# Kernel tuning notes

Hardware: AMD Instinct MI355X
Metric: run time of the kernel (lower is better)

The kernel has to match this reference:

```python
import jax, jax.numpy as jnp
import numpy as np

N = 50000       # nodes
E = 500000      # edges (before self-loops)
F_IN = 128      # node feature dim
F_E = 16        # edge feature dim
H = 8           # heads (conv1, conv2)
C1 = 32         # 256 // 8
C2 = 16         # 128 // 8
OUT = 1         # conv3 output channels (1 head, concat=False)
NS = 0.2        # leaky_relu negative slope
EPS = 1e-5      # batchnorm eps


def setup_inputs() -> dict:
    key = jax.random.key(0)
    ks = jax.random.split(key, 32)
    r = lambda k, s: jax.random.normal(k, s, jnp.float32) * 0.1
    inp = {
        'x': jax.random.normal(ks[0], (N, F_IN), jnp.float32),
        'edge_index': jax.random.randint(ks[1], (2, E), 0, N, jnp.int32),
        'edge_attr': jax.random.normal(ks[2], (E, F_E), jnp.float32),
        # conv1 (share_weights=True -> single lin)
        'W1': r(ks[3], (F_IN, H * C1)), 'b1': jnp.zeros((H * C1,), jnp.float32),
        'We1': r(ks[4], (F_E, H * C1)), 'att1': r(ks[5], (H, C1)),
        'bo1': jnp.zeros((H * C1,), jnp.float32),
        'g1': jnp.ones((H * C1,), jnp.float32), 'bt1': jnp.zeros((H * C1,), jnp.float32),
        # conv2 (share_weights=True)
        'W2': r(ks[6], (H * C1, H * C2)), 'b2': jnp.zeros((H * C2,), jnp.float32),
        'We2': r(ks[7], (F_E, H * C2)), 'att2': r(ks[8], (H, C2)),
        'bo2': jnp.zeros((H * C2,), jnp.float32),
        'g2': jnp.ones((H * C2,), jnp.float32), 'bt2': jnp.zeros((H * C2,), jnp.float32),
        # conv3 (share_weights=False -> separate lin_l / lin_r; 1 head, concat=False)
        'W3l': r(ks[9], (H * C2, OUT)), 'b3l': jnp.zeros((OUT,), jnp.float32),
        'W3r': r(ks[10], (H * C2, OUT)), 'b3r': jnp.zeros((OUT,), jnp.float32),
        'We3': r(ks[11], (F_E, OUT)), 'att3': r(ks[12], (1, OUT)),
        'bo3': jnp.zeros((OUT,), jnp.float32),
    }
    return inp


def _gatv2(x, src, dst, eattr, Wl, bl, Wr, br, We, att, bo, heads, ch, concat):
    """One GATv2Conv layer (PyG semantics), edges already include self-loops."""
    n = x.shape[0]
    xl = (x @ Wl + bl).reshape(n, heads, ch)              # source transform
    xr = (x @ Wr + br).reshape(n, heads, ch)              # target transform
    e = (eattr @ We).reshape(-1, heads, ch)               # edge transform (no bias)
    m = xl[src] + xr[dst] + e                             # [Etot, H, C]
    logit = jnp.einsum('ehc,hc->eh', jax.nn.leaky_relu(m, NS), att)
    lmax = jax.ops.segment_max(logit, dst, num_segments=n)
    ex = jnp.exp(logit - lmax[dst])
    denom = jax.ops.segment_sum(ex, dst, num_segments=n)
    alpha = ex / (denom[dst] + 1e-16)                     # segment softmax over dst
    out = jax.ops.segment_sum(alpha[:, :, None] * xl[src], dst, num_segments=n)
    out = out.reshape(n, heads * ch) if concat else out.mean(axis=1)
    return out + bo


def _bn(x, g, b):
    mu = x.mean(axis=0)
    var = ((x - mu) ** 2).mean(axis=0)
    return g * (x - mu) * jax.lax.rsqrt(var + EPS) + b


def reference(x, edge_index, edge_attr, W1, b1, We1, att1, bo1, g1, bt1,
              W2, b2, We2, att2, bo2, g2, bt2,
              W3l, b3l, W3r, b3r, We3, att3, bo3):
    n = x.shape[0]
    # add_self_loops=True with fill_value='mean' for edge_attr (PyG default)
    loop = jnp.arange(n, dtype=edge_index.dtype)
    src = jnp.concatenate([edge_index[0], loop])
    dst = jnp.concatenate([edge_index[1], loop])
    ea = jnp.concatenate([edge_attr,
                          jnp.broadcast_to(edge_attr.mean(axis=0), (n, edge_attr.shape[1]))], axis=0)

    h = _gatv2(x, src, dst, ea, W1, b1, W1, b1, We1, att1, bo1, H, C1, True)
    h = jax.nn.elu(_bn(h, g1, bt1))
    h = _gatv2(h, src, dst, ea, W2, b2, W2, b2, We2, att2, bo2, H, C2, True)
    h = jax.nn.elu(_bn(h, g2, bt2))
    out = _gatv2(h, src, dst, ea, W3l, b3l, W3r, b3r, We3, att3, bo3, 1, OUT, False)
    return out  # [N, 1]
```

## Files before the change

### kernel.cpp

```cpp
#include <hip/hip_runtime.h>

typedef unsigned short u16;
typedef __attribute__((ext_vector_type(4))) float f32x4;
typedef __attribute__((ext_vector_type(2))) float f32x2;
typedef __attribute__((ext_vector_type(8))) short bf16x8;

constexpr int Nn  = 50000;
constexpr int Ee  = 500000;
constexpr int ET  = Nn + Ee;
constexpr int FIN = 128;
constexpr int FE  = 16;
constexpr int Hh  = 8;
constexpr int C1  = 32, HC1 = 256;
constexpr int C2  = 16, HC2 = 128;
constexpr float NS  = 0.2f;
constexpr float EPS = 1e-5f;
constexpr float LOG2E = 1.44269504088896340736f;
constexpr int ATTN_BLOCKS = 2048;
constexpr int NWAVES = ATTN_BLOCKS * 4;

__device__ __forceinline__ float b2f(u16 u) { return __uint_as_float(((unsigned)u) << 16); }
__device__ __forceinline__ u16 f2b(float f) {
  unsigned u = __float_as_uint(f);
  u += 0x7FFF + ((u >> 16) & 1);
  return (u16)(u >> 16);
}

template <int RED>
__device__ __forceinline__ float red_sum(float v) {
  v += __int_as_float(__builtin_amdgcn_update_dpp(0, __float_as_int(v), 0xB1, 0xF, 0xF, true));
  v += __int_as_float(__builtin_amdgcn_update_dpp(0, __float_as_int(v), 0x4E, 0xF, 0xF, true));
  v += __int_as_float(__builtin_amdgcn_update_dpp(0, __float_as_int(v), 0x141, 0xF, 0xF, true));
  if constexpr (RED == 16)
    v += __int_as_float(__builtin_amdgcn_update_dpp(0, __float_as_int(v), 0x140, 0xF, 0xF, true));
  return v;
}

__global__ void k_init(int* __restrict__ deg, int* __restrict__ cursor, float* __restrict__ ea_mean) {
  int t = blockIdx.x * 256 + threadIdx.x;
  int stride = gridDim.x * 256;
  for (int i = t; i < Nn; i += stride) { deg[i] = 0; cursor[i] = 0; }
  if (t < FE) ea_mean[t] = 0.f;
}

__global__ void k_deg_mean(const int* __restrict__ ei, const float* __restrict__ ea,
                           int* __restrict__ deg, float* __restrict__ ea_mean) {
  int t = threadIdx.x;
  int e = blockIdx.x * 256 + t;
  if (e < ET) {
    int d = (e < Ee) ? ei[Ee + e] : (e - Ee);
    if ((unsigned)d >= (unsigned)Nn) d = 0;
    atomicAdd(&deg[d], 1);
  }
  __shared__ float s[256];
  int f  = t & 15;
  int r0 = (t >> 4) + blockIdx.x * 16;
  float acc = 0.f;
  for (int r = r0; r < Ee; r += gridDim.x * 16) acc += ea[r * FE + f];
  s[t] = acc;
  __syncthreads();
  if (t < 16) {
    float v = 0.f;
    for (int r = 0; r < 16; r++) v += s[r * 16 + t];
    atomicAdd(&ea_mean[t], v * (1.f / Ee));
  }
}

__global__ __launch_bounds__(1024) void k_scan(const int* __restrict__ deg, int* __restrict__ rowptr) {
  const int T = 1024;
  int t = threadIdx.x;
  const int CH = (Nn + T - 1) / T;
  int base = t * CH;
  int sum = 0;
  for (int i = 0; i < CH; i++) {
    int idx = base + i;
    if (idx < Nn) sum += deg[idx];
  }
  __shared__ int s[T];
  s[t] = sum;
  __syncthreads();
  for (int off = 1; off < T; off <<= 1) {
    int v = (t >= off) ? s[t - off] : 0;
    __syncthreads();
    s[t] += v;
    __syncthreads();
  }
  int run = (t == 0) ? 0 : s[t - 1];
  for (int i = 0; i < CH; i++) {
    int idx = base + i;
    if (idx < Nn) { rowptr[idx] = run; run += deg[idx]; }
  }
  if (t == T - 1) rowptr[Nn] = run;
}

__global__ void k_scatter(const int* __restrict__ ei, const int* __restrict__ rowptr,
                          int* __restrict__ cursor, int2* __restrict__ epack) {
  int e = blockIdx.x * 256 + threadIdx.x;
  if (e >= ET) return;
  if (e < 4) epack[ET + e] = make_int2(0, Ee);
  int s, d;
  if (e < Ee) { s = ei[e]; d = ei[Ee + e]; } else { s = d = e - Ee; }
  if ((unsigned)s >= (unsigned)Nn) s = 0;
  if ((unsigned)d >= (unsigned)Nn) d = 0;
  int pos = rowptr[d] + atomicAdd(&cursor[d], 1);
  epack[pos] = make_int2(s, e);
}

template <int WPN>
__global__ __launch_bounds__(256) void k_bn_coef_red(
    const float4* __restrict__ bnpart, const float* __restrict__ g,
    const float* __restrict__ bt, float2* __restrict__ coef) {
  constexpr int NW = NWAVES / WPN;
  int b = blockIdx.x;
  int w = b >> 6, lane = b & 63;
  int t = threadIdx.x;
  float4 s = make_float4(0.f, 0.f, 0.f, 0.f);
  for (int k = t; k < NW; k += 256) {
    float4 p = bnpart[(size_t)(k * WPN + w) * 64 + lane];
    s.x += p.x; s.y += p.y; s.z += p.z; s.w += p.w;
  }
  __shared__ float4 red[256];
  red[t] = s;
  __syncthreads();
  for (int off = 128; off > 0; off >>= 1) {
    if (t < off) {
      float4 o = red[t + off];
      red[t].x += o.x; red[t].y += o.y; red[t].z += o.z; red[t].w += o.w;
    }
    __syncthreads();
  }
  if (t == 0) {
    float4 tot = red[0];
    int c0 = w * 128 + lane * 2;
    float mu0 = tot.x * (1.f / Nn);
    float var0 = tot.y * (1.f / Nn) - mu0 * mu0;
    float sc0 = g[c0] * rsqrtf(var0 + EPS);
    coef[c0] = make_float2(sc0, bt[c0] - sc0 * mu0);
    float mu1 = tot.z * (1.f / Nn);
    float var1 = tot.w * (1.f / Nn) - mu1 * mu1;
    float sc1 = g[c0 + 1] * rsqrtf(var1 + EPS);
    coef[c0 + 1] = make_float2(sc1, bt[c0 + 1] - sc1 * mu1);
  }
}

template <int KK, int NN, typename AT, bool FUSE>
__global__ __launch_bounds__(256) void k_gemm_mfma(const AT* __restrict__ A, const float* __restrict__ W,
                                                   const float* __restrict__ bias, u16* __restrict__ C,
                                                   const float2* __restrict__ coef, int M) {
  int nblk = gridDim.x;
  int n = blockIdx.x;
  int q = nblk >> 3, r = nblk & 7;
  int xcd = n & 7, idx = n >> 3;
  int np = (xcd < r ? xcd * (q + 1) : r * (q + 1) + (xcd - r) * q) + idx;
  constexpr int XB = NN / 64;
  int col0 = (np % XB) * 64;
  int row0 = (np / XB) * 64;

  constexpr int WT = KK + 8;
  __shared__ u16 Wt[64 * WT];
  int tid = threadIdx.x;
  for (int idx2 = tid; idx2 < KK * 64; idx2 += 256) {
    int k = idx2 >> 6, c = idx2 & 63;
    Wt[c * WT + k] = f2b(W[(size_t)k * NN + col0 + c]);
  }
  __syncthreads();
  int lane = tid & 63;
  int w = tid >> 6;
  int mr = lane & 15, quad = lane >> 4;
  int row = row0 + w * 16 + mr;
  f32x4 acc[4];
#pragma unroll
  for (int t = 0; t < 4; t++) acc[t] = (f32x4){0.f, 0.f, 0.f, 0.f};
  union Frag { bf16x8 v; u16 u[8]; };
  for (int kb = 0; kb < KK; kb += 32) {
    Frag a;
    if (row < M) {
      if constexpr (sizeof(AT) == 4) {
        const float* ap = (const float*)&A[(size_t)row * KK + kb + quad * 8];
        float4 a0 = *reinterpret_cast<const float4*>(ap);
        float4 a1 = *reinterpret_cast<const float4*>(ap + 4);
        a.u[0] = f2b(a0.x); a.u[1] = f2b(a0.y); a.u[2] = f2b(a0.z); a.u[3] = f2b(a0.w);
        a.u[4] = f2b(a1.x); a.u[5] = f2b(a1.y); a.u[6] = f2b(a1.z); a.u[7] = f2b(a1.w);
      } else {
        a.v = *reinterpret_cast<const bf16x8*>(&A[(size_t)row * KK + kb + quad * 8]);
        if constexpr (FUSE) {
          int k0 = kb + quad * 8;
#pragma unroll
          for (int j = 0; j < 8; j++) {
            float2 c2 = coef[k0 + j];
            float y = b2f(a.u[j]) * c2.x + c2.y;
            y = y > 0.f ? y : __expf(y) - 1.f;
            a.u[j] = f2b(y);
          }
        }
      }
    } else {
#pragma unroll
      for (int j = 0; j < 8; j++) a.u[j] = 0;
    }
#pragma unroll
    for (int t = 0; t < 4; t++) {
      const bf16x8* bp = reinterpret_cast<const bf16x8*>(&Wt[(t * 16 + mr) * WT + kb + quad * 8]);
      acc[t] = __builtin_amdgcn_mfma_f32_16x16x32_bf16(a.v, *bp, acc[t], 0, 0, 0);
    }
  }
  int orow = row0 + w * 16 + quad * 4;
#pragma unroll
  for (int t = 0; t < 4; t++) {
    int col = col0 + t * 16 + mr;
    float bs = bias[col];
#pragma unroll
    for (int r2 = 0; r2 < 4; r2++) {
      int rr = orow + r2;
      if (rr < M) C[(size_t)rr * NN + col] = f2b(acc[t][r2] + bs);
    }
  }
}

template <int HC, int C, int WPN>
__global__ __launch_bounds__(256) void k_node_attn(
    const int* __restrict__ rowptr, const int2* __restrict__ epack,
    const u16* __restrict__ xl, const float* __restrict__ We, const float* __restrict__ att,
    const float* __restrict__ edge_attr, const float* __restrict__ ea_mean,
    const float* __restrict__ bo, u16* __restrict__ out,
    float4* __restrict__ bnpart) {
  __shared__ float sea[4][2][4][16];
  int lane = threadIdx.x & 63;
  int widx = threadIdx.x >> 6;
  int gwid = (blockIdx.x << 2) + widx;
  int nwaves = gridDim.x << 2;
  int w = gwid % WPN;
  int i0 = gwid / WPN;
  int istride = nwaves / WPN;
  int c0 = w * 128 + lane * 2;
  f32x2 w2[FE];
#pragma unroll
  for (int k = 0; k < FE; k++) {
    float2 t = *reinterpret_cast<const float2*>(&We[k * HC + c0]);
    w2[k] = (f32x2){t.x, t.y};
  }
  float at0 = att[c0] * LOG2E, at1 = att[c0 + 1] * LOG2E;
  f32x2 ews2 = {0.f, 0.f};
#pragma unroll
  for (int k = 0; k < FE; k++) ews2 += ea_mean[k] * w2[k];
  float b0 = bo[c0], b1 = bo[c0 + 1];
  constexpr int RED = C / 2;
  constexpr int UN = 4;

  auto stage = [&](const int2* sep, int buf) {
    int y01 = (lane & 4) ? sep[1].y : sep[0].y;
    int y23 = (lane & 4) ? sep[3].y : sep[2].y;
    int eidv = (lane & 8) ? y23 : y01;
    int ec = (eidv < Ee) ? eidv : 0;
    const float* src = edge_attr + (size_t)ec * FE + (lane & 3) * 4;
    if (lane < 16) {
      __builtin_amdgcn_global_load_lds(
          (const __attribute__((address_space(1))) unsigned int*)src,
          (__attribute__((address_space(3))) unsigned int*)&sea[widx][buf][0][0],
          16, 0, 0);
    }
  };
  auto ea_dot_lds = [&](int eid, int buf, int jj) -> f32x2 {
    if (eid < Ee) {
      const float4* ep = reinterpret_cast<const float4*>(&sea[widx][buf][jj][0]);
      f32x2 a = {0.f, 0.f};
#pragma unroll
      for (int k4 = 0; k4 < 4; k4++) {
        float4 u = ep[k4];
        a += u.x * w2[4 * k4 + 0];
        a += u.y * w2[4 * k4 + 1];
        a += u.z * w2[4 * k4 + 2];
        a += u.w * w2[4 * k4 + 3];
      }
      return a;
    }
    return ews2;
  };

  float bs0 = 0.f, bq0 = 0.f, bs1 = 0.f, bq1 = 0.f;
  if (i0 >= Nn) {
    bnpart[(size_t)gwid * 64 + lane] = make_float4(0.f, 0.f, 0.f, 0.f);
    return;
  }
  int p0 = __builtin_amdgcn_readfirstlane(rowptr[i0]);
  int p1 = __builtin_amdgcn_readfirstlane(rowptr[i0 + 1]);
  ushort2 xdr = *reinterpret_cast<const ushort2*>(&xl[(size_t)i0 * HC + c0]);

  for (int i = i0; i < Nn;) {
    int inext = i + istride;
    int np0 = 0, np1 = 0;
    ushort2 nxdr = make_ushort2(0, 0);
    if (inext < Nn) {
      np0 = __builtin_amdgcn_readfirstlane(rowptr[inext]);
      np1 = __builtin_amdgcn_readfirstlane(rowptr[inext + 1]);
      nxdr = *reinterpret_cast<const ushort2*>(&xl[(size_t)inext * HC + c0]);
    }
    f32x2 xd = (f32x2){b2f(xdr.x), b2f(xdr.y)};
    int nb = (p1 - p0 + UN - 1) >> 2;
    float m = -1e30f, l = 0.f;
    f32x2 acc = {0.f, 0.f};

    int2 se[UN];
#pragma unroll
    for (int j = 0; j < UN; j++) se[j] = epack[p0 + j];
    stage(se, 0);

    int pb = p0;
    for (int b = 0; b < nb; b++) {
      int buf = b & 1;
      asm volatile("s_waitcnt vmcnt(0)" ::: "memory");
      int sA[UN], eA[UN];
#pragma unroll
      for (int j = 0; j < UN; j++) {
        sA[j] = __builtin_amdgcn_readfirstlane(se[j].x);
        eA[j] = __builtin_amdgcn_readfirstlane(se[j].y);
      }
      ushort2 xr[UN];
#pragma unroll
      for (int j = 0; j < UN; j++)
        xr[j] = *reinterpret_cast<const ushort2*>(&xl[(size_t)sA[j] * HC + c0]);
      int pn = pb + UN;
      bool more = pn < p1;
      if (more) {
#pragma unroll
        for (int j = 0; j < UN; j++) se[j] = epack[pn + j];
      }
      f32x2 xs[UN];
      float part[UN];
#pragma unroll
      for (int j = 0; j < UN; j++) {
        f32x2 ew = ea_dot_lds(eA[j], buf, j);
        xs[j] = (f32x2){b2f(xr[j].x), b2f(xr[j].y)};
        f32x2 t = xs[j] + xd + ew;
        f32x2 tn = t * NS;
        float lk0 = fmaxf(t.x, tn.x), lk1 = fmaxf(t.y, tn.y);
        float pt = lk0 * at0 + lk1 * at1;
        pt = red_sum<RED>(pt);
        part[j] = (pb + j < p1) ? pt : -1e30f;
      }
      if (more) stage(se, buf ^ 1);
      float mn = m;
#pragma unroll
      for (int j = 0; j < UN; j++) mn = fmaxf(mn, part[j]);
      float sc = __builtin_amdgcn_exp2f(m - mn);
      float a[UN], asum = 0.f;
      f32x2 ax = {0.f, 0.f};
#pragma unroll
      for (int j = 0; j < UN; j++) {
        a[j] = __builtin_amdgcn_exp2f(part[j] - mn);
        asum += a[j];
        ax += a[j] * xs[j];
      }
      l = l * sc + asum;
      acc = acc * sc + ax;
      m = mn;
      pb = pn;
    }
    float inv = 1.f / (l + 1e-16f);
    f32x2 v = {acc.x * inv + b0, acc.y * inv + b1};
    u16 r0 = f2b(v.x), r1 = f2b(v.y);
    ushort2 ru; ru.x = r0; ru.y = r1;
    *reinterpret_cast<ushort2*>(&out[(size_t)i * HC + c0]) = ru;
    float v0 = b2f(r0), v1 = b2f(r1);
    bs0 += v0; bq0 += v0 * v0; bs1 += v1; bq1 += v1 * v1;
    i = inext; p0 = np0; p1 = np1; xdr = nxdr;
  }
  bnpart[(size_t)gwid * 64 + lane] = make_float4(bs0, bq0, bs1, bq1);
}

__global__ __launch_bounds__(256) void k_gemv3(const u16* __restrict__ h2,
                                               const float2* __restrict__ coef,
                                               const float* __restrict__ W3l, const float* __restrict__ b3l,
                                               const float* __restrict__ W3r, const float* __restrict__ b3r,
                                               float* __restrict__ xl3, float* __restrict__ xr3) {
  int lane = threadIdx.x & 63;
  int i = (blockIdx.x << 2) + (threadIdx.x >> 6);
  if (i >= Nn) return;
  float2 ca = coef[lane], cb = coef[64 + lane];
  float a = b2f(h2[(long)i * HC2 + lane]) * ca.x + ca.y;
  a = a > 0.f ? a : __expf(a) - 1.f;
  float b = b2f(h2[(long)i * HC2 + 64 + lane]) * cb.x + cb.y;
  b = b > 0.f ? b : __expf(b) - 1.f;
  float pl = a * W3l[lane] + b * W3l[64 + lane];
  float pr = a * W3r[lane] + b * W3r[64 + lane];
  for (int o = 1; o < 64; o <<= 1) { pl += __shfl_xor(pl, o); pr += __shfl_xor(pr, o); }
  if (lane == 0) { xl3[i] = pl + b3l[0]; xr3[i] = pr + b3r[0]; }
}

__global__ __launch_bounds__(256) void k_final3(
    const int* __restrict__ rowptr, const int2* __restrict__ epack,
    const float* __restrict__ xl3, const float* __restrict__ xr3,
    const float* __restrict__ We3, const float* __restrict__ att3,
    const float* __restrict__ edge_attr, const float* __restrict__ ea_mean,
    const float* __restrict__ bo3, float* __restrict__ out) {
  int t = threadIdx.x;
  int lane16 = t & 15;
  int i = blockIdx.x * 16 + (t >> 4);
  if (i >= Nn) return;
  float we[FE];
#pragma unroll
  for (int k4 = 0; k4 < 4; k4++) {
    float4 u = reinterpret_cast<const float4*>(We3)[k4];
    we[4 * k4] = u.x; we[4 * k4 + 1] = u.y; we[4 * k4 + 2] = u.z; we[4 * k4 + 3] = u.w;
  }
  float at = att3[0];
  float ews = 0.f;
#pragma unroll
  for (int k = 0; k < FE; k++) ews += ea_mean[k] * we[k];
  float xd = xr3[i];
  int p0 = rowptr[i], p1 = rowptr[i + 1];
  float m = -1e30f, l = 0.f, o = 0.f;
  for (int p = p0 + lane16; p < p1; p += 16) {
    int2 se = epack[p];
    int s = se.x, eid = se.y;
    float ew;
    if (eid < Ee) {
      const float4* ep = reinterpret_cast<const float4*>(&edge_attr[(size_t)eid * FE]);
      ew = 0.f;
#pragma unroll
      for (int k4 = 0; k4 < 4; k4++) {
        float4 u = ep[k4];
        ew += u.x * we[4 * k4] + u.y * we[4 * k4 + 1] + u.z * we[4 * k4 + 2] + u.w * we[4 * k4 + 3];
      }
    } else ew = ews;
    float xsv = xl3[s];
    float tt = xsv + xd + ew;
    float v = tt > 0.f ? tt : NS * tt;
    float logit = v * at;
    float mn = fmaxf(m, logit);
    float sc = __expf(m - mn);
    float a = __expf(logit - mn);
    l = l * sc + a;
    o = o * sc + a * xsv;
    m = mn;
  }
  float M = m;
#pragma unroll
  for (int off = 1; off < 16; off <<= 1) M = fmaxf(M, __shfl_xor(M, off));
  float adj = __expf(m - M);
  float lw = l * adj, ow = o * adj;
#pragma unroll
  for (int off = 1; off < 16; off <<= 1) { lw += __shfl_xor(lw, off); ow += __shfl_xor(ow, off); }
  if (lane16 == 0) out[i] = ow / (lw + 1e-16f) + bo3[0];
}

extern "C" void kernel_launch(void* const* d_in, const int* in_sizes, int n_in,
                              void* d_out, int out_size, void* d_ws, size_t ws_size,
                              hipStream_t stream) {
  const float* x    = (const float*)d_in[0];
  const int*   ei   = (const int*)d_in[1];
  const float* ea   = (const float*)d_in[2];
  const float* W1   = (const float*)d_in[3];
  const float* b1   = (const float*)d_in[4];
  const float* We1  = (const float*)d_in[5];
  const float* att1 = (const float*)d_in[6];
  const float* bo1  = (const float*)d_in[7];
  const float* g1   = (const float*)d_in[8];
  const float* bt1  = (const float*)d_in[9];
  const float* W2   = (const float*)d_in[10];
  const float* b2   = (const float*)d_in[11];
  const float* We2  = (const float*)d_in[12];
  const float* att2 = (const float*)d_in[13];
  const float* bo2  = (const float*)d_in[14];
  const float* g2   = (const float*)d_in[15];
  const float* bt2  = (const float*)d_in[16];
  const float* W3l  = (const float*)d_in[17];
  const float* b3l  = (const float*)d_in[18];
  const float* W3r  = (const float*)d_in[19];
  const float* b3r  = (const float*)d_in[20];
  const float* We3  = (const float*)d_in[21];
  const float* att3 = (const float*)d_in[22];
  const float* bo3  = (const float*)d_in[23];
  float* out = (float*)d_out;

  char* ws = (char*)d_ws;
  size_t off = 0;
  auto alloc = [&](size_t bytes) -> void* {
    void* p = ws + off;
    off = (off + bytes + 255) & ~(size_t)255;
    return p;
  };
  int*    deg     = (int*)alloc((size_t)Nn * 4);
  int*    rowptr  = (int*)alloc((size_t)(Nn + 1) * 4);
  int*    cursor  = (int*)alloc((size_t)Nn * 4);
  int2*   epack   = (int2*)alloc((size_t)(ET + 4) * 8);
  float*  ea_mean = (float*)alloc((size_t)FE * 4);
  float2* bncoef  = (float2*)alloc(256 * 8);
  float*  xl3     = (float*)alloc((size_t)Nn * 4);
  float*  xr3     = (float*)alloc((size_t)Nn * 4);
  u16*    xlA     = (u16*)alloc((size_t)Nn * 256 * 2);
  u16*    hB      = (u16*)alloc((size_t)Nn * 256 * 2);
  float4* bnpart  = (float4*)alloc((size_t)NWAVES * 64 * 16);

  k_init<<<512, 256, 0, stream>>>(deg, cursor, ea_mean);
  k_deg_mean<<<(ET + 255) / 256, 256, 0, stream>>>(ei, ea, deg, ea_mean);
  k_scan<<<1, 1024, 0, stream>>>(deg, rowptr);
  k_scatter<<<(ET + 255) / 256, 256, 0, stream>>>(ei, rowptr, cursor, epack);

  const int RB = (Nn + 63) / 64;

  k_gemm_mfma<FIN, HC1, float, false><<<(HC1 / 64) * RB, 256, 0, stream>>>(
      x, W1, b1, xlA, nullptr, Nn);
  k_node_attn<HC1, C1, 2><<<ATTN_BLOCKS, 256, 0, stream>>>(rowptr, epack, xlA, We1, att1,
                                                           ea, ea_mean, bo1, hB, bnpart);
  k_bn_coef_red<2><<<128, 256, 0, stream>>>(bnpart, g1, bt1, bncoef);

  k_gemm_mfma<HC1, HC2, u16, true><<<(HC2 / 64) * RB, 256, 0, stream>>>(
      hB, W2, b2, xlA, bncoef, Nn);
  k_node_attn<HC2, C2, 1><<<ATTN_BLOCKS, 256, 0, stream>>>(rowptr, epack, xlA, We2, att2,
                                                           ea, ea_mean, bo2, hB, bnpart);
  k_bn_coef_red<1><<<64, 256, 0, stream>>>(bnpart, g2, bt2, bncoef);

  k_gemv3<<<(Nn + 3) / 4, 256, 0, stream>>>(hB, bncoef, W3l, b3l, W3r, b3r, xl3, xr3);
  k_final3<<<(Nn + 15) / 16, 256, 0, stream>>>(rowptr, epack, xl3, xr3, We3, att3,
                                               ea, ea_mean, bo3, out);
}
```

Before: 646.0 us.

## Precompute conv3 edge projections and deepen edge-index prefetch in attention

The conv3 edge term (edge_attr · We3) is now computed once per edge inside the degree/mean pass and stored as a scalar array. The final kernel then reads one float per edge instead of gathering 64 bytes of edge features. The attention kernel prefetches edge-index packs two blocks ahead and stages the next block's edge features earlier, so index loads overlap with the gathers. The epack padding is enlarged to cover the deeper prefetch, and the row pointers are no longer forced to scalar registers at load time. This adds a 2 MB workspace array plus extra registers in the attention loop.

```diff
diff --git a/kernel.cpp b/kernel.cpp
--- a/kernel.cpp
+++ b/kernel.cpp
@@ -18,6 +18,7 @@
 constexpr float LOG2E = 1.44269504088896340736f;
 constexpr int ATTN_BLOCKS = 2048;
 constexpr int NWAVES = ATTN_BLOCKS * 4;
+constexpr int EPAD = 12;
 
 __device__ __forceinline__ float b2f(u16 u) { return __uint_as_float(((unsigned)u) << 16); }
 __device__ __forceinline__ u16 f2b(float f) {
@@ -44,7 +45,9 @@
 }
 
 __global__ void k_deg_mean(const int* __restrict__ ei, const float* __restrict__ ea,
-                           int* __restrict__ deg, float* __restrict__ ea_mean) {
+                           const float* __restrict__ We3,
+                           int* __restrict__ deg, float* __restrict__ ea_mean,
+                           float* __restrict__ ew3) {
   int t = threadIdx.x;
   int e = blockIdx.x * 256 + t;
   if (e < ET) {
@@ -54,9 +57,15 @@
   }
   __shared__ float s[256];
   int f  = t & 15;
+  float w3 = We3[f];
   int r0 = (t >> 4) + blockIdx.x * 16;
   float acc = 0.f;
-  for (int r = r0; r < Ee; r += gridDim.x * 16) acc += ea[r * FE + f];
+  for (int r = r0; r < Ee; r += gridDim.x * 16) {
+    float v = ea[r * FE + f];
+    acc += v;
+    float d3 = red_sum<16>(v * w3);
+    if (f == 0) ew3[r] = d3;
+  }
   s[t] = acc;
   __syncthreads();
   if (t < 16) {
@@ -97,7 +106,7 @@
                           int* __restrict__ cursor, int2* __restrict__ epack) {
   int e = blockIdx.x * 256 + threadIdx.x;
   if (e >= ET) return;
-  if (e < 4) epack[ET + e] = make_int2(0, Ee);
+  if (e < EPAD) epack[ET + e] = make_int2(0, Ee);
   int s, d;
   if (e < Ee) { s = ei[e]; d = ei[Ee + e]; } else { s = d = e - Ee; }
   if ((unsigned)s >= (unsigned)Nn) s = 0;
@@ -282,8 +291,7 @@
     bnpart[(size_t)gwid * 64 + lane] = make_float4(0.f, 0.f, 0.f, 0.f);
     return;
   }
-  int p0 = __builtin_amdgcn_readfirstlane(rowptr[i0]);
-  int p1 = __builtin_amdgcn_readfirstlane(rowptr[i0 + 1]);
+  int p0 = rowptr[i0], p1 = rowptr[i0 + 1];
   ushort2 xdr = *reinterpret_cast<const ushort2*>(&xl[(size_t)i0 * HC + c0]);
 
   for (int i = i0; i < Nn;) {
@@ -291,8 +299,8 @@
     int np0 = 0, np1 = 0;
     ushort2 nxdr = make_ushort2(0, 0);
     if (inext < Nn) {
-      np0 = __builtin_amdgcn_readfirstlane(rowptr[inext]);
-      np1 = __builtin_amdgcn_readfirstlane(rowptr[inext + 1]);
+      np0 = rowptr[inext];
+      np1 = rowptr[inext + 1];
       nxdr = *reinterpret_cast<const ushort2*>(&xl[(size_t)inext * HC + c0]);
     }
     f32x2 xd = (f32x2){b2f(xdr.x), b2f(xdr.y)};
@@ -300,30 +308,35 @@
     float m = -1e30f, l = 0.f;
     f32x2 acc = {0.f, 0.f};
 
-    int2 se[UN];
-#pragma unroll
-    for (int j = 0; j < UN; j++) se[j] = epack[p0 + j];
-    stage(se, 0);
+    int2 seC[UN], seN[UN];
+#pragma unroll
+    for (int j = 0; j < UN; j++) seC[j] = epack[p0 + j];
+    stage(seC, 0);
+#pragma unroll
+    for (int j = 0; j < UN; j++) seN[j] = epack[p0 + UN + j];
 
     int pb = p0;
     for (int b = 0; b < nb; b++) {
       int buf = b & 1;
       asm volatile("s_waitcnt vmcnt(0)" ::: "memory");
+      int pn = pb + UN;
+      bool more = pn < p1;
+      if (more) stage(seN, buf ^ 1);
       int sA[UN], eA[UN];
 #pragma unroll
       for (int j = 0; j < UN; j++) {
-        sA[j] = __builtin_amdgcn_readfirstlane(se[j].x);
-        eA[j] = __builtin_amdgcn_readfirstlane(se[j].y);
+        sA[j] = __builtin_amdgcn_readfirstlane(seC[j].x);
+        eA[j] = __builtin_amdgcn_readfirstlane(seC[j].y);
       }
       ushort2 xr[UN];
 #pragma unroll
       for (int j = 0; j < UN; j++)
         xr[j] = *reinterpret_cast<const ushort2*>(&xl[(size_t)sA[j] * HC + c0]);
-      int pn = pb + UN;
-      bool more = pn < p1;
+#pragma unroll
+      for (int j = 0; j < UN; j++) seC[j] = seN[j];
       if (more) {
 #pragma unroll
-        for (int j = 0; j < UN; j++) se[j] = epack[pn + j];
+        for (int j = 0; j < UN; j++) seN[j] = epack[pn + UN + j];
       }
       f32x2 xs[UN];
       float part[UN];
@@ -338,7 +351,6 @@
         pt = red_sum<RED>(pt);
         part[j] = (pb + j < p1) ? pt : -1e30f;
       }
-      if (more) stage(se, buf ^ 1);
       float mn = m;
 #pragma unroll
       for (int j = 0; j < UN; j++) mn = fmaxf(mn, part[j]);
@@ -391,38 +403,23 @@
     const int* __restrict__ rowptr, const int2* __restrict__ epack,
     const float* __restrict__ xl3, const float* __restrict__ xr3,
     const float* __restrict__ We3, const float* __restrict__ att3,
-    const float* __restrict__ edge_attr, const float* __restrict__ ea_mean,
+    const float* __restrict__ ew3, const float* __restrict__ ea_mean,
     const float* __restrict__ bo3, float* __restrict__ out) {
   int t = threadIdx.x;
   int lane16 = t & 15;
   int i = blockIdx.x * 16 + (t >> 4);
   if (i >= Nn) return;
-  float we[FE];
-#pragma unroll
-  for (int k4 = 0; k4 < 4; k4++) {
-    float4 u = reinterpret_cast<const float4*>(We3)[k4];
-    we[4 * k4] = u.x; we[4 * k4 + 1] = u.y; we[4 * k4 + 2] = u.z; we[4 * k4 + 3] = u.w;
-  }
   float at = att3[0];
   float ews = 0.f;
 #pragma unroll
-  for (int k = 0; k < FE; k++) ews += ea_mean[k] * we[k];
+  for (int k = 0; k < FE; k++) ews += ea_mean[k] * We3[k];
   float xd = xr3[i];
   int p0 = rowptr[i], p1 = rowptr[i + 1];
   float m = -1e30f, l = 0.f, o = 0.f;
   for (int p = p0 + lane16; p < p1; p += 16) {
     int2 se = epack[p];
     int s = se.x, eid = se.y;
-    float ew;
-    if (eid < Ee) {
-      const float4* ep = reinterpret_cast<const float4*>(&edge_attr[(size_t)eid * FE]);
-      ew = 0.f;
-#pragma unroll
-      for (int k4 = 0; k4 < 4; k4++) {
-        float4 u = ep[k4];
-        ew += u.x * we[4 * k4] + u.y * we[4 * k4 + 1] + u.z * we[4 * k4 + 2] + u.w * we[4 * k4 + 3];
-      }
-    } else ew = ews;
+    float ew = (eid < Ee) ? ew3[eid] : ews;
     float xsv = xl3[s];
     float tt = xsv + xd + ew;
     float v = tt > 0.f ? tt : NS * tt;
@@ -483,8 +480,9 @@
   int*    deg     = (int*)alloc((size_t)Nn * 4);
   int*    rowptr  = (int*)alloc((size_t)(Nn + 1) * 4);
   int*    cursor  = (int*)alloc((size_t)Nn * 4);
-  int2*   epack   = (int2*)alloc((size_t)(ET + 4) * 8);
+  int2*   epack   = (int2*)alloc((size_t)(ET + EPAD) * 8);
   float*  ea_mean = (float*)alloc((size_t)FE * 4);
+  float*  ew3     = (float*)alloc((size_t)Ee * 4);
   float2* bncoef  = (float2*)alloc(256 * 8);
   float*  xl3     = (float*)alloc((size_t)Nn * 4);
   float*  xr3     = (float*)alloc((size_t)Nn * 4);
@@ -493,7 +491,7 @@
   float4* bnpart  = (float4*)alloc((size_t)NWAVES * 64 * 16);
 
   k_init<<<512, 256, 0, stream>>>(deg, cursor, ea_mean);
-  k_deg_mean<<<(ET + 255) / 256, 256, 0, stream>>>(ei, ea, deg, ea_mean);
+  k_deg_mean<<<(ET + 255) / 256, 256, 0, stream>>>(ei, ea, We3, deg, ea_mean, ew3);
   k_scan<<<1, 1024, 0, stream>>>(deg, rowptr);
   k_scatter<<<(ET + 255) / 256, 256, 0, stream>>>(ei, rowptr, cursor, epack);
 
@@ -513,5 +511,5 @@
 
   k_gemv3<<<(Nn + 3) / 4, 256, 0, stream>>>(hB, bncoef, W3l, b3l, W3r, b3r, xl3, xr3);
   k_final3<<<(Nn + 15) / 16, 256, 0, stream>>>(rowptr, epack, xl3, xr3, We3, att3,
-                                               ea, ea_mean, bo3, out);
-}
+                                               ew3, ea_mean, bo3, out);
+}
```

Measured after the change: 650.7 us. No clear change (+0.7%).
